# Performance work log

Hardware: AMD Instinct MI355X
Metric: run time of the kernel (lower is better)

## Reference

```python
import jax, jax.numpy as jnp
import numpy as np

NUM_HEADS = 16
HEAD_DIM = 64
HIDDEN = NUM_HEADS * HEAD_DIM  # 1024
B, T = 32, 512


def setup_inputs() -> dict:
    key = jax.random.key(0)
    ks = jax.random.split(key, 10)
    s = 1.0 / np.sqrt(HIDDEN)
    inp = {
        "x": jax.random.normal(ks[0], (B, HIDDEN, T), dtype=jnp.float32),
        "mask": jax.random.randint(ks[1], (B, T), 0, 2, dtype=jnp.int32),
        "Wq": jax.random.uniform(ks[2], (HIDDEN, HIDDEN), jnp.float32, -s, s),
        "bq": jax.random.uniform(ks[3], (HIDDEN,), jnp.float32, -s, s),
        "Wk": jax.random.uniform(ks[4], (HIDDEN, HIDDEN), jnp.float32, -s, s),
        "bk": jax.random.uniform(ks[5], (HIDDEN,), jnp.float32, -s, s),
        "Wv": jax.random.uniform(ks[6], (HIDDEN, HIDDEN), jnp.float32, -s, s),
        "bv": jax.random.uniform(ks[7], (HIDDEN,), jnp.float32, -s, s),
        "Wo": jax.random.uniform(ks[8], (HIDDEN, HIDDEN), jnp.float32, -s, s),
        "bo": jax.random.uniform(ks[9], (HIDDEN,), jnp.float32, -s, s),
    }
    return inp


def reference(x, mask, Wq, bq, Wk, bk, Wv, bv, Wo, bo):
    # x: [B, hidden, T] -> tokens along last axis
    b, h, t = x.shape
    xt = jnp.swapaxes(x, 1, 2)  # [B, T, hidden]

    def heads(w, bias):
        y = xt @ w.T + bias                       # [B, T, hidden]
        return y.reshape(b, t, NUM_HEADS, HEAD_DIM).transpose(0, 2, 1, 3)  # [B, nh, T, hd]

    q = heads(Wq, bq)
    k = heads(Wk, bk)
    v = heads(Wv, bv)

    scores = jnp.einsum("bhqd,bhkd->bhqk", q, k) / jnp.sqrt(jnp.float32(HEAD_DIM))
    # masked_fill(mask==0, -inf) then clamp to [-50, 50]: masked entries become -50
    scores = jnp.where(mask[:, None, None, :] == 0, -jnp.inf, scores)
    scores = jnp.clip(scores, -50.0, 50.0)
    attn = jax.nn.softmax(scores, axis=-1)        # [B, nh, T, T]
    out = jnp.einsum("bhqk,bhkd->bhqd", attn, v)  # [B, nh, T, hd]
    out = out.transpose(0, 2, 1, 3).reshape(b, t, h)
    out = out @ Wo.T + bo                         # [B, T, hidden]
    return out.max(axis=1)                        # [B, hidden]
```

## Files before the change

### kernel.cpp

```cpp
#include <hip/hip_runtime.h>


typedef _Float16 half8 __attribute__((ext_vector_type(8)));
typedef _Float16 half4 __attribute__((ext_vector_type(4)));
typedef float floatx4 __attribute__((ext_vector_type(4)));
typedef unsigned uintx2 __attribute__((ext_vector_type(2)));

#define HID 1024
#define TT 512
#define NB 32
#define QSCALE 0.1803368801111244f
#define SB2 72.13475204444817f

__device__ __forceinline__ void gload16(const void* g, void* l) {
    __builtin_amdgcn_global_load_lds(
        (const __attribute__((address_space(1))) unsigned int*)g,
        (__attribute__((address_space(3))) unsigned int*)l, 16, 0, 0);
}

__device__ __forceinline__ unsigned fkey(float f) {
    unsigned u = __float_as_uint(f);
    return (u & 0x80000000u) ? ~u : (u | 0x80000000u);
}
__device__ __forceinline__ float funkey(unsigned k) {
    unsigned u = (k & 0x80000000u) ? (k ^ 0x80000000u) : ~k;
    return __uint_as_float(u);
}

__global__ __launch_bounds__(256) void prep_kernel(
    const float* __restrict__ Wq, const float* __restrict__ Wk,
    const float* __restrict__ Wv, const float* __restrict__ Wo,
    _Float16* __restrict__ Wcat,
    const float* __restrict__ x, _Float16* __restrict__ xT,
    unsigned* __restrict__ omax,
    const float* __restrict__ bq, float* __restrict__ bqs)
{
    __shared__ float tile[64][65];
    const int bid = blockIdx.x;
    if (bid < 4096) {
        int i4 = bid * 256 + threadIdx.x;
        int sec = i4 >> 18;
        int off4 = i4 & ((1 << 18) - 1);
        const float* src = (sec == 0) ? Wq : (sec == 1) ? Wk
                          : (sec == 2) ? Wv : Wo;
        float4 v = ((const float4*)src)[off4];
        if (sec == 0) {
            v.x *= QSCALE; v.y *= QSCALE; v.z *= QSCALE; v.w *= QSCALE;
        }
        half4 h = {(_Float16)v.x, (_Float16)v.y, (_Float16)v.z, (_Float16)v.w};
        *(half4*)(Wcat + (size_t)i4 * 4) = h;
    } else if (bid < 8192) {
        int idx = bid - 4096;
        int b = idx >> 7, h0 = ((idx >> 3) & 15) * 64, t0 = (idx & 7) * 64;
        int tx = threadIdx.x & 15, ty = threadIdx.x >> 4;
        const float* xb = x + ((size_t)b * HID + h0) * TT + t0;
        for (int p = 0; p < 4; p++) {
            int r = ty + 16 * p;
            float4 v = *(const float4*)(xb + (size_t)r * TT + tx * 4);
            tile[r][tx * 4 + 0] = v.x;
            tile[r][tx * 4 + 1] = v.y;
            tile[r][tx * 4 + 2] = v.z;
            tile[r][tx * 4 + 3] = v.w;
        }
        __syncthreads();
        int hc = (threadIdx.x & 7) * 8, tb = threadIdx.x >> 3;
        for (int rd = 0; rd < 2; rd++) {
            int tt = tb + 32 * rd;
            half8 pk;
            for (int k = 0; k < 8; k++)
                pk[k] = (_Float16)tile[hc + k][tt];
            *(half8*)(xT + ((size_t)b * TT + t0 + tt) * HID + h0 + hc) = pk;
        }
    } else if (bid < 8320) {
        omax[(bid - 8192) * 256 + threadIdx.x] = 0u;
    } else {
        int i = (bid - 8320) * 256 + threadIdx.x;
        bqs[i] = bq[i] * QSCALE;
    }
}

#define PH_PRE do { \
    __builtin_amdgcn_s_barrier(); \
    asm volatile("s_waitcnt lgkmcnt(0)" ::: "memory"); \
    __builtin_amdgcn_sched_barrier(0); \
    __builtin_amdgcn_s_setprio(1); \
} while (0)

#define PH_POST(N) do { \
    __builtin_amdgcn_s_setprio(0); \
    asm volatile("s_waitcnt vmcnt(" #N ")" ::: "memory"); \
    __builtin_amdgcn_s_barrier(); \
} while (0)

#define LDA(P, MH) do { \
    const _Float16* ab_ = lds + (P) * 16384 + (MH) * 8192 + aoff; \
    af[0][0] = *(const half8*)(ab_ + pb0); \
    af[0][1] = *(const half8*)(ab_ + pb1); \
    af[1][0] = *(const half8*)(ab_ + 1024 + pb0); \
    af[1][1] = *(const half8*)(ab_ + 1024 + pb1); \
    af[2][0] = *(const half8*)(ab_ + 2048 + pb0); \
    af[2][1] = *(const half8*)(ab_ + 2048 + pb1); \
    af[3][0] = *(const half8*)(ab_ + 3072 + pb0); \
    af[3][1] = *(const half8*)(ab_ + 3072 + pb1); \
} while (0)

#define LDB(P, NH) do { \
    const _Float16* bb_ = lds + 32768 + (P) * 16384 + (NH) * 8192 + boff; \
    bf[NH][0][0] = *(const half8*)(bb_ + pb0); \
    bf[NH][0][1] = *(const half8*)(bb_ + pb1); \
    bf[NH][1][0] = *(const half8*)(bb_ + 1024 + pb0); \
    bf[NH][1][1] = *(const half8*)(bb_ + 1024 + pb1); \
} while (0)

#define MFMAQ(MH, NH) do { \
    _Pragma("unroll") \
    for (int j_ = 0; j_ < 4; ++j_) { \
        _Pragma("unroll") \
        for (int n_ = 0; n_ < 2; ++n_) { \
            floatx4 c_ = acc[(MH) * 4 + j_][(NH) * 2 + n_]; \
            c_ = __builtin_amdgcn_mfma_f32_16x16x32_f16( \
                af[j_][0], bf[NH][n_][0], c_, 0, 0, 0); \
            c_ = __builtin_amdgcn_mfma_f32_16x16x32_f16( \
                af[j_][1], bf[NH][n_][1], c_, 0, 0, 0); \
            acc[(MH) * 4 + j_][(NH) * 2 + n_] = c_; \
        } \
    } \
} while (0)

#define STAGE_A(P, MH, K0) do { \
    _Float16* d_ = lds + (P) * 16384 + (MH) * 8192 + wst; \
    gload16(ag + (MH) * 65536 + (K0), d_); \
    gload16(ag + 131072 + (MH) * 65536 + (K0), d_ + 4096); \
} while (0)

#define STAGE_B(P, NH, K0) do { \
    _Float16* d_ = lds + 32768 + (P) * 16384 + (NH) * 8192 + wst; \
    gload16(bg + (NH) * 32768 + (K0), d_); \
    gload16(bg + 131072 + (NH) * 32768 + (K0), d_ + 4096); \
} while (0)

__device__ __forceinline__ void mainloop256(
    const _Float16* __restrict__ Ag,
    const _Float16* __restrict__ Bg,
    _Float16* lds, floatx4 acc[8][4], int tid)
{
    const int lane = tid & 63;
    const int w = tid >> 6, wr = w >> 2, wc = w & 3;
    const int l15 = lane & 15, quad = lane >> 4;
    const int pa = quad ^ (l15 & 7);
    const int pb0 = pa * 8, pb1 = (pa ^ 4) * 8;
    const int aoff = (wr * 64 + l15) * 64;
    const int boff = (wc * 32 + l15) * 64;
    const int wst = w * 512;
    const int r = tid >> 3;
    const int sg = (tid & 7) ^ (r & 7);
    const int nbase = ((r >> 5) << 6) + (r & 31);
    const _Float16* ag = Ag + (size_t)r * 1024 + sg * 8;
    const _Float16* bg = Bg + (size_t)nbase * 1024 + sg * 8;

    half8 af[4][2], bf[2][2][2];

    STAGE_A(0, 0, 0); STAGE_B(0, 0, 0); STAGE_B(0, 1, 0); STAGE_A(0, 1, 0);
    STAGE_A(1, 0, 64); STAGE_B(1, 0, 64); STAGE_B(1, 1, 64);
    asm volatile("s_waitcnt vmcnt(10)" ::: "memory");
    __builtin_amdgcn_s_barrier();

    for (int i = 0; i < 7; ++i) {
        const int kb = i * 128 + 64;
        const int kn0 = kb + 64, kn1 = kb + 128;
        LDA(0, 0); LDB(0, 0); STAGE_A(1, 1, kb);
        PH_PRE; MFMAQ(0, 0); PH_POST(10);
        LDB(0, 1);            STAGE_A(0, 0, kn0);
        PH_PRE; MFMAQ(0, 1); PH_POST(10);
        LDA(0, 1);            STAGE_B(0, 0, kn0);
        PH_PRE; MFMAQ(1, 1); PH_POST(10);
                              STAGE_B(0, 1, kn0);
        PH_PRE; MFMAQ(1, 0); PH_POST(10);
        LDA(1, 0); LDB(1, 0); STAGE_A(0, 1, kn0);
        PH_PRE; MFMAQ(0, 0); PH_POST(10);
        LDB(1, 1);            STAGE_A(1, 0, kn1);
        PH_PRE; MFMAQ(0, 1); PH_POST(10);
        LDA(1, 1);            STAGE_B(1, 0, kn1);
        PH_PRE; MFMAQ(1, 1); PH_POST(10);
                              STAGE_B(1, 1, kn1);
        PH_PRE; MFMAQ(1, 0); PH_POST(10);
    }
    LDA(0, 0); LDB(0, 0); STAGE_A(1, 1, 960);
    PH_PRE; MFMAQ(0, 0); PH_POST(10);
    LDB(0, 1);
    PH_PRE; MFMAQ(0, 1); PH_POST(8);
    LDA(0, 1);
    PH_PRE; MFMAQ(1, 1); PH_POST(6);
    PH_PRE; MFMAQ(1, 0); PH_POST(4);
    LDA(1, 0); LDB(1, 0);
    PH_PRE; MFMAQ(0, 0); PH_POST(2);
    LDB(1, 1);
    PH_PRE; MFMAQ(0, 1); PH_POST(0);
    LDA(1, 1);
    PH_PRE; MFMAQ(1, 1); MFMAQ(1, 0);
    __builtin_amdgcn_s_setprio(0);
}

#define AOF(J) (((J) >> 4) * 262144 + ((J) & 15) * 64)
#define BOF(J) (((J) & 15) * 64)

#define SA1(P, MH, J) do { \
    _Float16* d_ = lds + (P) * 16384 + (MH) * 8192 + wst; \
    gload16(ag + (MH) * 65536 + AOF(J), d_); \
    gload16(ag + 131072 + (MH) * 65536 + AOF(J), d_ + 4096); \
} while (0)

#define SB1(P, NH, J) do { \
    _Float16* d_ = lds + 32768 + (P) * 16384 + (NH) * 8192 + wst; \
    gload16(bg + (NH) * 32768 + BOF(J), d_); \
    gload16(bg + 131072 + (NH) * 32768 + BOF(J), d_ + 4096); \
} while (0)

#define PAIR(I) do { \
    const int j1 = 2 * (I) + 1, j2 = 2 * (I) + 2, j3 = 2 * (I) + 3; \
    LDA(0, 0); LDB(0, 0); SA1(1, 1, j1); \
    PH_PRE; MFMAQ(0, 0); PH_POST(10); \
    LDB(0, 1);            SA1(0, 0, j2); \
    PH_PRE; MFMAQ(0, 1); PH_POST(10); \
    LDA(0, 1);            SB1(0, 0, j2); \
    PH_PRE; MFMAQ(1, 1); PH_POST(10); \
                          SB1(0, 1, j2); \
    PH_PRE; MFMAQ(1, 0); PH_POST(10); \
    LDA(1, 0); LDB(1, 0); SA1(0, 1, j2); \
    PH_PRE; MFMAQ(0, 0); PH_POST(10); \
    LDB(1, 1);            SA1(1, 0, j3); \
    PH_PRE; MFMAQ(0, 1); PH_POST(10); \
    LDA(1, 1);            SB1(1, 0, j3); \
    PH_PRE; MFMAQ(1, 1); PH_POST(10); \
                          SB1(1, 1, j3); \
    PH_PRE; MFMAQ(1, 0); PH_POST(10); \
} while (0)

__global__ __launch_bounds__(512, 2) void gemm1_kernel(
    const _Float16* __restrict__ Wcat,
    const float* __restrict__ bqs, const float* __restrict__ bk,
    const float* __restrict__ bv,
    const _Float16* __restrict__ xT,
    _Float16* __restrict__ QT, _Float16* __restrict__ KT,
    _Float16* __restrict__ Vb)
{
    __shared__ __align__(16) _Float16 smem[65536];
    _Float16* lds = smem;
    const int tid = threadIdx.x;
    const int id = blockIdx.x;
    const int xcd = id & 7, slot = id >> 3;
    const int grp = xcd + 8 * (slot >> 2);
    const int mseg = slot & 3;
    const int n0 = (grp & 1) * 256;
    const int bb = grp >> 1;
    const int lane = tid & 63;
    const int w = tid >> 6, wr = w >> 2, wc = w & 3;
    const int l15 = lane & 15, quad = lane >> 4;
    const int pa = quad ^ (l15 & 7);
    const int pb0 = pa * 8, pb1 = (pa ^ 4) * 8;
    const int aoff = (wr * 64 + l15) * 64;
    const int boff = (wc * 32 + l15) * 64;
    const int wst = w * 512;
    const int r = tid >> 3;
    const int sg = (tid & 7) ^ (r & 7);
    const int nbase = ((r >> 5) << 6) + (r & 31);
    const _Float16* ag = Wcat + (size_t)(mseg * 768 + r) * 1024 + sg * 8;
    const _Float16* bg = xT + ((size_t)bb * TT + n0 + nbase) * 1024 + sg * 8;

    floatx4 acc[8][4] = {};
    half8 af[4][2], bf[2][2][2];

    auto epi = [&](int v) {
        const int mt = mseg * 3 + v;
        const int sec = mt >> 2;
        const int mo = (mt & 3) * 256 + wr * 128;
        if (sec < 2) {
            const float* bias = (sec == 0) ? bqs : bk;
            _Float16* dst = (sec == 0) ? QT : KT;
            _Float16* drow = dst + ((size_t)bb * TT + n0 + wc * 64 + l15) * HID
                             + mo + quad * 4;
            for (int mi = 0; mi < 8; ++mi) {
                float bs[4];
                for (int rr = 0; rr < 4; ++rr)
                    bs[rr] = bias[mo + mi * 16 + quad * 4 + rr];
                for (int ni = 0; ni < 4; ++ni) {
                    half4 pk;
                    for (int rr = 0; rr < 4; ++rr)
                        pk[rr] = (_Float16)(acc[mi][ni][rr] + bs[rr]);
                    *(half4*)(drow + (size_t)(ni * 16) * HID + mi * 16) = pk;
                    acc[mi][ni] = (floatx4){0.f, 0.f, 0.f, 0.f};
                }
            }
        } else {
            for (int mi = 0; mi < 8; ++mi) {
                float bs[4];
                for (int rr = 0; rr < 4; ++rr)
                    bs[rr] = bv[mo + mi * 16 + quad * 4 + rr];
                for (int ni = 0; ni < 4; ++ni) {
                    int t = n0 + wc * 64 + ni * 16 + l15;
                    for (int rr = 0; rr < 4; ++rr) {
                        int o = mo + mi * 16 + quad * 4 + rr;
                        Vb[((size_t)bb * HID + o) * TT + t] =
                            (_Float16)(acc[mi][ni][rr] + bs[rr]);
                    }
                    acc[mi][ni] = (floatx4){0.f, 0.f, 0.f, 0.f};
                }
            }
        }
    };

    SA1(0, 0, 0); SB1(0, 0, 0); SB1(0, 1, 0); SA1(0, 1, 0);
    SA1(1, 0, 1); SB1(1, 0, 1); SB1(1, 1, 1);
    asm volatile("s_waitcnt vmcnt(10)" ::: "memory");
    __builtin_amdgcn_s_barrier();

    for (int ii = 0; ii < 8; ++ii) PAIR(ii);
    epi(0);
    for (int ii = 8; ii < 16; ++ii) PAIR(ii);
    epi(1);
    for (int ii = 16; ii < 23; ++ii) PAIR(ii);
    LDA(0, 0); LDB(0, 0); SA1(1, 1, 47);
    PH_PRE; MFMAQ(0, 0); PH_POST(10);
    LDB(0, 1);
    PH_PRE; MFMAQ(0, 1); PH_POST(8);
    LDA(0, 1);
    PH_PRE; MFMAQ(1, 1); PH_POST(6);
    PH_PRE; MFMAQ(1, 0); PH_POST(4);
    LDA(1, 0); LDB(1, 0);
    PH_PRE; MFMAQ(0, 0); PH_POST(2);
    LDB(1, 1);
    PH_PRE; MFMAQ(0, 1); PH_POST(0);
    LDA(1, 1);
    PH_PRE; MFMAQ(1, 1); MFMAQ(1, 0);
    __builtin_amdgcn_s_setprio(0);
    epi(2);
}

__global__ __launch_bounds__(256) void attn_kernel(
    const _Float16* __restrict__ QT, const _Float16* __restrict__ KT,
    const _Float16* __restrict__ Vb, const int* __restrict__ mask,
    _Float16* __restrict__ OcT)
{
    __shared__ __align__(16) _Float16 kvbuf[4 * 4096];
    __shared__ __align__(16) _Float16 ps[2 * 4096];
    __shared__ __align__(16) float msf[2][64];

    const int id = blockIdx.x;
    const int xcd = id & 7, slot = id >> 3;
    const int grp = xcd + 8 * (slot >> 2);
    const int q0 = (slot & 3) * 128;
    const int hd = grp & 15, b = grp >> 4;
    const int tid = threadIdx.x;
    const int lane = tid & 63, wid = tid >> 6;
    const int l15 = lane & 15, quad = lane >> 4;

    const _Float16* QTb = QT + ((size_t)b * TT + q0) * HID + hd * 64;
    const _Float16* KTb = KT + (size_t)b * TT * HID + hd * 64;
    const _Float16* Vbb = Vb + ((size_t)b * HID + hd * 64) * TT;
    const int* mb = mask + b * TT;

    const int srow = lane >> 3;
    const int sg = (lane & 7) ^ srow;
    const int pa = quad ^ (l15 & 7);
    const int pz = l15 & 7;

    for (int qt = 0; qt < 2; qt++)
        for (int p = 0; p < 2; p++) {
            int r = p * 32 + wid * 8 + srow;
            gload16(QTb + (size_t)(qt * 64 + r) * HID + sg * 8,
                    kvbuf + qt * 4096 + (p * 32 + wid * 8) * 64);
        }
    __syncthreads();
    half8 bq[2][2];
    for (int qt = 0; qt < 2; qt++) {
        bq[qt][0] = *(half8*)(kvbuf + qt * 4096 + (wid * 16 + l15) * 64 + pa * 8);
        bq[qt][1] = *(half8*)(kvbuf + qt * 4096 + (wid * 16 + l15) * 64 + (pa ^ 4) * 8);
    }
    __syncthreads();

    auto stage = [&](int jcn, int bufn) {
        int t0n = jcn * 64;
        _Float16* kd = kvbuf + bufn * 4096;
        _Float16* vd = kvbuf + (2 + bufn) * 4096;
        for (int p = 0; p < 2; p++) {
            int r = p * 32 + wid * 8 + srow;
            gload16(KTb + (size_t)(t0n + r) * HID + sg * 8,
                    kd + (p * 32 + wid * 8) * 64);
            gload16(Vbb + (size_t)r * TT + t0n + sg * 8,
                    vd + (p * 32 + wid * 8) * 64);
        }
        if (tid < 64) msf[bufn][tid] = mb[t0n + tid] ? SB2 : -SB2;
    };

    stage(0, 0);

    floatx4 oacc[2][4] = {};
    float rs[2] = {0.f, 0.f};
    const float lo = -SB2;

    for (int jc = 0; jc < 8; jc++) {
        const int cur = jc & 1;
        __syncthreads();
        if (jc < 7) stage(jc + 1, 1 - cur);

        const _Float16* ks = kvbuf + cur * 4096;
        const _Float16* vs = kvbuf + (2 + cur) * 4096;

        for (int jt = 0; jt < 4; jt++) {
            half8 ka0 = *(half8*)(ks + (jt * 16 + l15) * 64 + pa * 8);
            half8 ka1 = *(half8*)(ks + (jt * 16 + l15) * 64 + (pa ^ 4) * 8);
            floatx4 hi = *(floatx4*)(&msf[cur][jt * 16 + quad * 4]);
            for (int qt = 0; qt < 2; qt++) {
                floatx4 sc = {0.f, 0.f, 0.f, 0.f};
                sc = __builtin_amdgcn_mfma_f32_16x16x32_f16(ka0, bq[qt][0], sc, 0, 0, 0);
                sc = __builtin_amdgcn_mfma_f32_16x16x32_f16(ka1, bq[qt][1], sc, 0, 0, 0);
                float e0 = __builtin_amdgcn_exp2f(fminf(fmaxf(sc[0], lo), hi[0]));
                float e1 = __builtin_amdgcn_exp2f(fminf(fmaxf(sc[1], lo), hi[1]));
                float e2 = __builtin_amdgcn_exp2f(fminf(fmaxf(sc[2], lo), hi[2]));
                float e3 = __builtin_amdgcn_exp2f(fminf(fmaxf(sc[3], lo), hi[3]));
                rs[qt] += (e0 + e1) + (e2 + e3);
                unsigned uA = __builtin_bit_cast(
                    unsigned, __builtin_amdgcn_cvt_pkrtz(e0, e1));
                unsigned uB = __builtin_bit_cast(
                    unsigned, __builtin_amdgcn_cvt_pkrtz(e2, e3));
                uintx2 uv = {uA, uB};
                half4 pk = __builtin_bit_cast(half4, uv);
                int g = jt * 2 + (quad >> 1);
                *(half4*)(ps + qt * 4096 + (wid * 16 + l15) * 64 + (g ^ pz) * 8 +
                          (quad & 1) * 4) = pk;
            }
        }
        for (int kc = 0; kc < 2; kc++) {
            int g = kc * 4 + quad;
            half8 bv8[4];
            for (int d4 = 0; d4 < 4; d4++)
                bv8[d4] = *(half8*)(vs + (d4 * 16 + l15) * 64 + (g ^ pz) * 8);
            for (int qt = 0; qt < 2; qt++) {
                half8 ap = *(half8*)(ps + qt * 4096 + (wid * 16 + l15) * 64 +
                                     (g ^ pz) * 8);
                for (int d4 = 0; d4 < 4; d4++)
                    oacc[qt][d4] = __builtin_amdgcn_mfma_f32_16x16x32_f16(
                        ap, bv8[d4], oacc[qt][d4], 0, 0, 0);
            }
        }
    }

    for (int qt = 0; qt < 2; qt++) {
        float s = rs[qt];
        s += __shfl_xor(s, 16, 64);
        s += __shfl_xor(s, 32, 64);
        s = 1.0f / s;
        float inv[4];
        for (int r = 0; r < 4; r++) inv[r] = __shfl(s, quad * 4 + r, 64);
        for (int d4 = 0; d4 < 4; d4++)
            for (int r = 0; r < 4; r++) {
                int t = q0 + qt * 64 + wid * 16 + quad * 4 + r;
                int c = hd * 64 + d4 * 16 + l15;
                OcT[((size_t)b * TT + t) * HID + c] =
                    (_Float16)(oacc[qt][d4][r] * inv[r]);
            }
    }
}

__global__ __launch_bounds__(512, 2) void gemm2_kernel(
    const _Float16* __restrict__ Wo16, const _Float16* __restrict__ OcT,
    unsigned* __restrict__ omax)
{
    __shared__ __align__(16) _Float16 smem[65536];
    _Float16* lds = smem;
    const int tid = threadIdx.x;
    const int id = blockIdx.x;
    const int xcd = id & 7, slot = id >> 3;
    const int grp = xcd + 8 * (slot >> 2);
    const int m0 = (slot & 3) * 256;
    const int n0 = (grp & 1) * 256;
    const int bb = grp >> 1;
    const int lane = tid & 63;
    const int w = tid >> 6, wr = w >> 2;
    const int l15 = lane & 15, quad = lane >> 4;

    floatx4 acc[8][4] = {};
    mainloop256(Wo16 + (size_t)m0 * 1024,
                OcT + ((size_t)bb * TT + n0) * HID, lds, acc, tid);

    for (int mi = 0; mi < 8; ++mi)
        for (int rr = 0; rr < 4; ++rr) {
            float v = acc[mi][0][rr];
            v = fmaxf(v, acc[mi][1][rr]);
            v = fmaxf(v, acc[mi][2][rr]);
            v = fmaxf(v, acc[mi][3][rr]);
            for (int d = 1; d < 16; d <<= 1)
                v = fmaxf(v, __shfl_xor(v, d, 64));
            if (l15 == 0) {
                int o = m0 + wr * 128 + mi * 16 + quad * 4 + rr;
                atomicMax(&omax[bb * HID + o], fkey(v));
            }
        }
}

__global__ __launch_bounds__(256) void final_kernel(
    const unsigned* __restrict__ omax, const float* __restrict__ bo,
    float* __restrict__ out)
{
    int i = blockIdx.x * 256 + threadIdx.x;
    out[i] = funkey(omax[i]) + bo[i & 1023];
}

extern "C" void kernel_launch(void* const* d_in, const int* in_sizes, int n_in,
                              void* d_out, int out_size, void* d_ws, size_t ws_size,
                              hipStream_t stream)
{
    const float* x  = (const float*)d_in[0];
    const int* mask = (const int*)d_in[1];
    const float* Wq = (const float*)d_in[2];
    const float* bq = (const float*)d_in[3];
    const float* Wk = (const float*)d_in[4];
    const float* bk = (const float*)d_in[5];
    const float* Wv = (const float*)d_in[6];
    const float* bv = (const float*)d_in[7];
    const float* Wo = (const float*)d_in[8];
    const float* bo = (const float*)d_in[9];
    float* out = (float*)d_out;

    char* ws = (char*)d_ws;
    _Float16* Wcat = (_Float16*)(ws);
    _Float16* xT   = (_Float16*)(ws + (8ull  << 20));
    _Float16* QT   = (_Float16*)(ws + (40ull << 20));
    _Float16* KT   = (_Float16*)(ws + (72ull << 20));
    _Float16* Vb   = (_Float16*)(ws + (104ull << 20));
    _Float16* OcT  = (_Float16*)(ws + (136ull << 20));
    unsigned* omax = (unsigned*)(ws + (168ull << 20));
    float*    bqs  = (float*)(ws + (168ull << 20) + (128ull << 10));

    prep_kernel<<<8324, 256, 0, stream>>>(Wq, Wk, Wv, Wo, Wcat, x, xT, omax,
                                          bq, bqs);
    gemm1_kernel<<<256, 512, 0, stream>>>(Wcat, bqs, bk, bv, xT, QT, KT, Vb);
    attn_kernel<<<2048, 256, 0, stream>>>(QT, KT, Vb, mask, OcT);
    gemm2_kernel<<<256, 512, 0, stream>>>(Wcat + (3ull << 20), OcT, omax);
    final_kernel<<<128, 256, 0, stream>>>(omax, bo, out);
}
```

Before: 315.8 us.

## Remap gemm1 M-segments so each block emits Q, K, V for one slice, staging stores through LDS

Each block now computes the same 256-row slice of Q, K and V (stride between sections in Wcat) instead of three consecutive 256-row tiles, so every block follows an identical Q→K→V epilogue sequence. Q/K epilogues stage fp16 results through a per-wave LDS scratch region with a swizzle, then write coalesced 16-byte rows. Bias vectors are preloaded into registers, and the iteration after each epilogue uses larger vmcnt waits to absorb the extra store traffic. Costs are more LDS (an extra scratch area), more live registers, and the risk that the changed wait counts or layout mapping are off.

```diff
diff --git a/kernel.cpp b/kernel.cpp
--- a/kernel.cpp
+++ b/kernel.cpp
@@ -201,7 +201,7 @@
     __builtin_amdgcn_s_setprio(0);
 }
 
-#define AOF(J) (((J) >> 4) * 262144 + ((J) & 15) * 64)
+#define AOF(J) (((J) >> 4) * 1048576 + ((J) & 15) * 64)
 #define BOF(J) (((J) & 15) * 64)
 
 #define SA1(P, MH, J) do { \
@@ -236,6 +236,26 @@
     PH_PRE; MFMAQ(1, 0); PH_POST(10); \
 } while (0)
 
+#define PAIR_EPI(I) do { \
+    const int j1 = 2 * (I) + 1, j2 = 2 * (I) + 2, j3 = 2 * (I) + 3; \
+    LDA(0, 0); LDB(0, 0); SA1(1, 1, j1); \
+    PH_PRE; MFMAQ(0, 0); PH_POST(26); \
+    LDB(0, 1);            SA1(0, 0, j2); \
+    PH_PRE; MFMAQ(0, 1); PH_POST(26); \
+    LDA(0, 1);            SB1(0, 0, j2); \
+    PH_PRE; MFMAQ(1, 1); PH_POST(26); \
+                          SB1(0, 1, j2); \
+    PH_PRE; MFMAQ(1, 0); PH_POST(26); \
+    LDA(1, 0); LDB(1, 0); SA1(0, 1, j2); \
+    PH_PRE; MFMAQ(0, 0); PH_POST(26); \
+    LDB(1, 1);            SA1(1, 0, j3); \
+    PH_PRE; MFMAQ(0, 1); PH_POST(10); \
+    LDA(1, 1);            SB1(1, 0, j3); \
+    PH_PRE; MFMAQ(1, 1); PH_POST(10); \
+                          SB1(1, 1, j3); \
+    PH_PRE; MFMAQ(1, 0); PH_POST(10); \
+} while (0)
+
 __global__ __launch_bounds__(512, 2) void gemm1_kernel(
     const _Float16* __restrict__ Wcat,
     const float* __restrict__ bqs, const float* __restrict__ bk,
@@ -244,7 +264,7 @@
     _Float16* __restrict__ QT, _Float16* __restrict__ KT,
     _Float16* __restrict__ Vb)
 {
-    __shared__ __align__(16) _Float16 smem[65536];
+    __shared__ __align__(16) _Float16 smem[73728];
     _Float16* lds = smem;
     const int tid = threadIdx.x;
     const int id = blockIdx.x;
@@ -264,46 +284,67 @@
     const int r = tid >> 3;
     const int sg = (tid & 7) ^ (r & 7);
     const int nbase = ((r >> 5) << 6) + (r & 31);
-    const _Float16* ag = Wcat + (size_t)(mseg * 768 + r) * 1024 + sg * 8;
+    const _Float16* ag = Wcat + (size_t)(mseg * 256 + r) * 1024 + sg * 8;
     const _Float16* bg = xT + ((size_t)bb * TT + n0 + nbase) * 1024 + sg * 8;
 
     floatx4 acc[8][4] = {};
     half8 af[4][2], bf[2][2][2];
 
-    auto epi = [&](int v) {
-        const int mt = mseg * 3 + v;
-        const int sec = mt >> 2;
-        const int mo = (mt & 3) * 256 + wr * 128;
-        if (sec < 2) {
-            const float* bias = (sec == 0) ? bqs : bk;
-            _Float16* dst = (sec == 0) ? QT : KT;
-            _Float16* drow = dst + ((size_t)bb * TT + n0 + wc * 64 + l15) * HID
-                             + mo + quad * 4;
-            for (int mi = 0; mi < 8; ++mi) {
-                float bs[4];
-                for (int rr = 0; rr < 4; ++rr)
-                    bs[rr] = bias[mo + mi * 16 + quad * 4 + rr];
-                for (int ni = 0; ni < 4; ++ni) {
+    floatx4 qb4[8], kb4[8];
+    {
+        const int mo = mseg * 256 + wr * 128 + quad * 4;
+#pragma unroll
+        for (int mi = 0; mi < 8; ++mi) {
+            qb4[mi] = *(const floatx4*)(bqs + mo + mi * 16);
+            kb4[mi] = *(const floatx4*)(bk  + mo + mi * 16);
+        }
+#pragma unroll
+        for (int mi = 0; mi < 8; ++mi)
+            asm volatile("" :: "v"(qb4[mi]), "v"(kb4[mi]));
+    }
+
+    auto epi_qk = [&](const floatx4* bias4, _Float16* dst) {
+        const int mo = mseg * 256 + wr * 128;
+        _Float16* scr = smem + 65536 + w * 1024;
+        for (int ni = 0; ni < 4; ++ni) {
+            for (int hf = 0; hf < 2; ++hf) {
+#pragma unroll
+                for (int mi4 = 0; mi4 < 4; ++mi4) {
+                    int mi = hf * 4 + mi4;
                     half4 pk;
+                    floatx4 bs = bias4[mi];
                     for (int rr = 0; rr < 4; ++rr)
                         pk[rr] = (_Float16)(acc[mi][ni][rr] + bs[rr]);
-                    *(half4*)(drow + (size_t)(ni * 16) * HID + mi * 16) = pk;
+                    int gs = ((mi4 << 1) | (quad >> 1)) ^ (l15 & 7);
+                    *(half4*)(scr + l15 * 64 + gs * 8 + (quad & 1) * 4) = pk;
                     acc[mi][ni] = (floatx4){0.f, 0.f, 0.f, 0.f};
                 }
+                asm volatile("s_waitcnt lgkmcnt(0)" ::: "memory");
+                _Float16* dr = dst +
+                    ((size_t)bb * TT + n0 + wc * 64 + ni * 16 + l15) * HID +
+                    mo + hf * 64;
+                const _Float16* srd = scr + l15 * 64;
+#pragma unroll
+                for (int it = 0; it < 2; ++it) {
+                    int c = quad + it * 4;
+                    uint4 vv = *(const uint4*)(srd + (c ^ (l15 & 7)) * 8);
+                    *(uint4*)(dr + c * 8) = vv;
+                }
+                asm volatile("s_waitcnt lgkmcnt(0)" ::: "memory");
             }
-        } else {
-            for (int mi = 0; mi < 8; ++mi) {
-                float bs[4];
-                for (int rr = 0; rr < 4; ++rr)
-                    bs[rr] = bv[mo + mi * 16 + quad * 4 + rr];
-                for (int ni = 0; ni < 4; ++ni) {
-                    int t = n0 + wc * 64 + ni * 16 + l15;
-                    for (int rr = 0; rr < 4; ++rr) {
-                        int o = mo + mi * 16 + quad * 4 + rr;
-                        Vb[((size_t)bb * HID + o) * TT + t] =
-                            (_Float16)(acc[mi][ni][rr] + bs[rr]);
-                    }
-                    acc[mi][ni] = (floatx4){0.f, 0.f, 0.f, 0.f};
+        }
+    };
+
+    auto epi_v = [&]() {
+        const int mo = mseg * 256 + wr * 128;
+        for (int mi = 0; mi < 8; ++mi) {
+            floatx4 bs = *(const floatx4*)(bv + mo + mi * 16 + quad * 4);
+            for (int ni = 0; ni < 4; ++ni) {
+                int t = n0 + wc * 64 + ni * 16 + l15;
+                for (int rr = 0; rr < 4; ++rr) {
+                    int o = mo + mi * 16 + quad * 4 + rr;
+                    Vb[((size_t)bb * HID + o) * TT + t] =
+                        (_Float16)(acc[mi][ni][rr] + bs[rr]);
                 }
             }
         }
@@ -315,10 +356,12 @@
     __builtin_amdgcn_s_barrier();
 
     for (int ii = 0; ii < 8; ++ii) PAIR(ii);
-    epi(0);
-    for (int ii = 8; ii < 16; ++ii) PAIR(ii);
-    epi(1);
-    for (int ii = 16; ii < 23; ++ii) PAIR(ii);
+    epi_qk(qb4, QT);
+    PAIR_EPI(8);
+    for (int ii = 9; ii < 16; ++ii) PAIR(ii);
+    epi_qk(kb4, KT);
+    PAIR_EPI(16);
+    for (int ii = 17; ii < 23; ++ii) PAIR(ii);
     LDA(0, 0); LDB(0, 0); SA1(1, 1, 47);
     PH_PRE; MFMAQ(0, 0); PH_POST(10);
     LDB(0, 1);
@@ -333,7 +376,7 @@
     LDA(1, 1);
     PH_PRE; MFMAQ(1, 1); MFMAQ(1, 0);
     __builtin_amdgcn_s_setprio(0);
-    epi(2);
+    epi_v();
 }
 
 __global__ __launch_bounds__(256) void attn_kernel(
```

Result: slower. 333.5 us (+5.6%).
